# Performance work log

Measured on AMD Instinct MI355X. Metric: run time of the kernel, lower is better.

The kernel has to match this reference:

```python
import jax, jax.numpy as jnp
import numpy as np

B, S, D = 4, 4096, 1024
STATE = 1024
HID = 4 * D
EPS_NORM = 1e-6           # RMSNorm module eps
EPS_FP32 = 1.1920929e-7   # torch F.rms_norm default eps = finfo(fp32).eps


def rms_norm(x, eps):
    # no learned weight (RMSNorm(dim=-1) has weight=None)
    return x * jax.lax.rsqrt(jnp.mean(jnp.square(x), axis=-1, keepdims=True) + eps)


def setup_inputs() -> dict:
    key = jax.random.key(0)
    ks = jax.random.split(key, 8)
    scale_d = 1.0 / np.sqrt(D)
    scale_s = 1.0 / np.sqrt(STATE)
    scale_h = 1.0 / np.sqrt(HID)
    return {
        "x": jax.random.normal(ks[0], (B, S, D), jnp.float32),
        "x0": jax.random.normal(ks[1], (B, S, D), jnp.float32),
        "Wu": jax.random.normal(ks[2], (STATE, D), jnp.float32) * scale_d,
        "Wg": jax.random.normal(ks[3], (STATE, D), jnp.float32) * scale_d,
        "Wo": jax.random.normal(ks[4], (D, STATE), jnp.float32) * scale_s,
        "Wfc": jax.random.normal(ks[5], (HID, D), jnp.float32) * scale_d,
        "Wproj": jax.random.normal(ks[6], (D, HID), jnp.float32) * scale_h,
        "memory_mix": jnp.ones((D,), jnp.float32),
        "mlp_scale": jnp.ones((D,), jnp.float32),
        "resid_mix": jnp.stack([jnp.ones((D,), jnp.float32), jnp.zeros((D,), jnp.float32)]),
    }


def reference(x, x0, Wu, Wg, Wo, Wfc, Wproj, memory_mix, mlp_scale, resid_mix):
    # residual mix of x and x0
    x = resid_mix[0][None, None, :] * x + resid_mix[1][None, None, :] * x0

    # --- CausalPrefixMemory branch ---
    h = rms_norm(x, EPS_NORM)
    update = jnp.einsum('bsd,kd->bsk', h, Wu)
    gate = jax.nn.sigmoid(jnp.einsum('bsd,kd->bsk', h, Wg))
    memory = jnp.cumsum(gate * update, axis=1)          # [B,S,STATE]
    denom = jnp.arange(1, S + 1, dtype=jnp.float32)[None, :, None]
    m = rms_norm(memory / denom, EPS_FP32)
    mem_out = jnp.einsum('bsk,dk->bsd', m, Wo)
    x = x + memory_mix[None, None, :] * mem_out

    # --- MLP branch: relu^2 ---
    h2 = rms_norm(x, EPS_NORM)
    r = jax.nn.relu(jnp.einsum('bsd,hd->bsh', h2, Wfc))
    mlp_out = jnp.einsum('bsh,dh->bsd', jnp.square(r), Wproj)
    x = x + mlp_scale[None, None, :] * mlp_out
    return x
```

## Files before the change

### kernel.cpp

```cpp
#include <hip/hip_runtime.h>
#include <stdint.h>

typedef unsigned short u16;
typedef __attribute__((ext_vector_type(8))) short s16x8;
typedef __attribute__((ext_vector_type(4))) float f32x4;

__device__ __forceinline__ u16 f2bf(float f) {
  uint32_t u = __float_as_uint(f);
  uint32_t r = (u + 0x7FFFu + ((u >> 16) & 1u)) >> 16;
  return (u16)r;
}

__device__ __forceinline__ void gll16(const void* g, void* lds) {
  __builtin_amdgcn_global_load_lds(
      (const __attribute__((address_space(1))) uint32_t*)g,
      (__attribute__((address_space(3))) uint32_t*)lds, 16, 0, 0);
}

__device__ __forceinline__ void xcd_swz(int& bx, int& by) {
  int gx = gridDim.x;
  int lin = blockIdx.y * gx + blockIdx.x;
  int cpx = (gx * gridDim.y) >> 3;
  int nl = (lin & 7) * cpx + (lin >> 3);
  bx = nl % gx;
  by = nl / gx;
}

__global__ __launch_bounds__(256) void k_f2b(const float* __restrict__ src,
                                             u16* __restrict__ dst, int n) {
  int i = (blockIdx.x * 256 + threadIdx.x) * 4;
  if (i < n) {
    float4 v = *(const float4*)(src + i);
    ushort4 o;
    o.x = f2bf(v.x); o.y = f2bf(v.y); o.z = f2bf(v.z); o.w = f2bf(v.w);
    *(ushort4*)(dst + i) = o;
  }
}

template <bool MIX>
__global__ __launch_bounds__(256) void k_rms(const float* __restrict__ X,
                                             const float* __restrict__ X0,
                                             const float* __restrict__ rmix,
                                             float* __restrict__ XMout,
                                             u16* __restrict__ Hout, float eps) {
  const int row = blockIdx.x, t = threadIdx.x;
  const size_t base = (size_t)row * 1024;
  float4 v;
  if (MIX) {
    float4 a = ((const float4*)(X + base))[t];
    float4 b = ((const float4*)(X0 + base))[t];
    float4 c0 = ((const float4*)rmix)[t];
    float4 c1 = ((const float4*)(rmix + 1024))[t];
    v.x = c0.x * a.x + c1.x * b.x;
    v.y = c0.y * a.y + c1.y * b.y;
    v.z = c0.z * a.z + c1.z * b.z;
    v.w = c0.w * a.w + c1.w * b.w;
  } else {
    v = ((const float4*)(X + base))[t];
  }
  float ss = v.x * v.x + v.y * v.y + v.z * v.z + v.w * v.w;
#pragma unroll
  for (int o = 32; o > 0; o >>= 1) ss += __shfl_xor(ss, o);
  __shared__ float red[4];
  if ((t & 63) == 0) red[t >> 6] = ss;
  __syncthreads();
  float tot = red[0] + red[1] + red[2] + red[3];
  float sc = rsqrtf(tot * (1.0f / 1024.0f) + eps);
  if (MIX) ((float4*)(XMout + base))[t] = v;
  ushort4 hv;
  hv.x = f2bf(v.x * sc); hv.y = f2bf(v.y * sc);
  hv.z = f2bf(v.z * sc); hv.w = f2bf(v.w * sc);
  ((ushort4*)(Hout + base))[t] = hv;
}

__global__ __launch_bounds__(256) void k_scan1(const float* __restrict__ P,
                                               float* __restrict__ CS) {
  int blk = blockIdx.x;
  int chunk = blk & 63, b = blk >> 6;
  const float4* p = (const float4*)(P + ((size_t)b * 4096 + chunk * 64) * 1024)
                    + threadIdx.x;
  float4 s = {0.f, 0.f, 0.f, 0.f};
#pragma unroll 8
  for (int i = 0; i < 64; ++i) {
    float4 v = p[(size_t)i * 256];
    s.x += v.x; s.y += v.y; s.z += v.z; s.w += v.w;
  }
  ((float4*)(CS + ((size_t)b * 64 + chunk) * 1024))[threadIdx.x] = s;
}

__global__ __launch_bounds__(256) void k_scan2(float* __restrict__ CS) {
  int idx = blockIdx.x * 256 + threadIdx.x;
  int b = idx >> 10, k = idx & 1023;
  float run = 0.f;
  for (int c = 0; c < 64; ++c) {
    size_t o = ((size_t)b * 64 + c) * 1024 + k;
    float v = CS[o];
    CS[o] = run;
    run += v;
  }
}

__global__ __launch_bounds__(256) void k_scan3f(const float* __restrict__ P,
                                                const float* __restrict__ CS,
                                                u16* __restrict__ Mout) {
  int blk = blockIdx.x;
  int chunk = blk & 63, b = blk >> 6;
  const int t = threadIdx.x, wid = t >> 6;
  __shared__ float red[2][4];
  float4 run = ((const float4*)(CS + ((size_t)b * 64 + chunk) * 1024))[t];
  const float4* p = (const float4*)(P + ((size_t)b * 4096 + chunk * 64) * 1024) + t;
  u16* mo = Mout + ((size_t)b * 4096 + chunk * 64) * 1024 + t * 4;
  for (int i = 0; i < 64; ++i) {
    float4 v = p[(size_t)i * 256];
    run.x += v.x; run.y += v.y; run.z += v.z; run.w += v.w;
    float inv = 1.0f / (float)(chunk * 64 + i + 1);
    float4 y;
    y.x = run.x * inv; y.y = run.y * inv; y.z = run.z * inv; y.w = run.w * inv;
    float ss = y.x * y.x + y.y * y.y + y.z * y.z + y.w * y.w;
#pragma unroll
    for (int o = 32; o > 0; o >>= 1) ss += __shfl_xor(ss, o);
    if ((t & 63) == 0) red[i & 1][wid] = ss;
    __syncthreads();
    float tot = red[i & 1][0] + red[i & 1][1] + red[i & 1][2] + red[i & 1][3];
    float sc = rsqrtf(tot * (1.0f / 1024.0f) + 1.1920929e-7f);
    ushort4 hv;
    hv.x = f2bf(y.x * sc); hv.y = f2bf(y.y * sc);
    hv.z = f2bf(y.z * sc); hv.w = f2bf(y.w * sc);
    *(ushort4*)(mo + (size_t)i * 1024) = hv;
  }
}

__global__ __launch_bounds__(256, 2) void gemm_dual(
    const u16* __restrict__ A, const u16* __restrict__ Bu,
    const u16* __restrict__ Bg, float* __restrict__ P, int K) {
  __shared__ __align__(16) u16 As[128 * 64];
  __shared__ __align__(16) u16 Us[64 * 64];
  __shared__ __align__(16) u16 Gs[64 * 64];
  const int t = threadIdx.x;
  const int lane = t & 63, wid = t >> 6;
  int bx, by;
  xcd_swz(bx, by);
  const int m0 = by * 128, n0 = bx * 64;
  const int wm = wid * 32;
  const int l15 = lane & 15, lhi = lane >> 4;

  size_t gA[4], gU[2];
#pragma unroll
  for (int i = 0; i < 4; ++i) {
    int j = i * 256 + t;
    int row = j >> 3;
    int k16 = (j & 7) ^ (row & 7);
    gA[i] = (size_t)(m0 + row) * K + k16 * 8;
  }
#pragma unroll
  for (int i = 0; i < 2; ++i) {
    int j = i * 256 + t;
    int row = j >> 3;
    int k16 = (j & 7) ^ (row & 7);
    gU[i] = (size_t)(n0 + row) * K + k16 * 8;
  }

  f32x4 au[2][4], ag[2][4];
#pragma unroll
  for (int mi = 0; mi < 2; ++mi)
#pragma unroll
    for (int ni = 0; ni < 4; ++ni) { au[mi][ni] = 0.0f; ag[mi][ni] = 0.0f; }

  for (int kb = 0; kb < K; kb += 64) {
#pragma unroll
    for (int i = 0; i < 4; ++i) {
      int j = i * 256 + t;
      gll16(A + gA[i] + kb, &As[j * 8]);
    }
#pragma unroll
    for (int i = 0; i < 2; ++i) {
      int j = i * 256 + t;
      gll16(Bu + gU[i] + kb, &Us[j * 8]);
      gll16(Bg + gU[i] + kb, &Gs[j * 8]);
    }
    __syncthreads();
#pragma unroll
    for (int kc = 0; kc < 2; ++kc) {
      s16x8 af[2], uf[4], gf[4];
#pragma unroll
      for (int mi = 0; mi < 2; ++mi) {
        int row = wm + mi * 16 + l15;
        int k16 = (kc * 4 + lhi) ^ (row & 7);
        af[mi] = *(const s16x8*)&As[row * 64 + k16 * 8];
      }
#pragma unroll
      for (int ni = 0; ni < 4; ++ni) {
        int row = ni * 16 + l15;
        int k16 = (kc * 4 + lhi) ^ (row & 7);
        uf[ni] = *(const s16x8*)&Us[row * 64 + k16 * 8];
        gf[ni] = *(const s16x8*)&Gs[row * 64 + k16 * 8];
      }
#pragma unroll
      for (int mi = 0; mi < 2; ++mi)
#pragma unroll
        for (int ni = 0; ni < 4; ++ni) {
          au[mi][ni] = __builtin_amdgcn_mfma_f32_16x16x32_bf16(
              af[mi], uf[ni], au[mi][ni], 0, 0, 0);
          ag[mi][ni] = __builtin_amdgcn_mfma_f32_16x16x32_bf16(
              af[mi], gf[ni], ag[mi][ni], 0, 0, 0);
        }
    }
    __syncthreads();
  }

#pragma unroll
  for (int mi = 0; mi < 2; ++mi) {
    int r0 = m0 + wm + mi * 16 + lhi * 4;
#pragma unroll
    for (int ni = 0; ni < 4; ++ni) {
      int c = n0 + ni * 16 + l15;
#pragma unroll
      for (int j = 0; j < 4; ++j) {
        float u = au[mi][ni][j], g = ag[mi][ni][j];
        P[(size_t)(r0 + j) * 1024 + c] = u / (1.0f + __expf(-g));
      }
    }
  }
}

template <int EPI>
__global__ __launch_bounds__(256, 2) void gemm_bf16(
    const u16* __restrict__ A, const u16* __restrict__ Bw, void* __restrict__ Cout,
    const float* __restrict__ Cadd, const float* __restrict__ colscale,
    int K, int lda, int ldb, int ldc) {
  __shared__ __align__(16) u16 As[128 * 64];
  __shared__ __align__(16) u16 Bs[128 * 64];
  const int t = threadIdx.x;
  const int lane = t & 63, wid = t >> 6;
  int bx, by;
  xcd_swz(bx, by);
  const int m0 = by * 128, n0 = bx * 128;
  const int wm = (wid >> 1) * 64, wn = (wid & 1) * 64;
  const int l15 = lane & 15, lhi = lane >> 4;

  size_t gA[4], gB[4];
#pragma unroll
  for (int i = 0; i < 4; ++i) {
    int j = i * 256 + t;
    int row = j >> 3;
    int k16 = (j & 7) ^ (row & 7);
    gA[i] = (size_t)(m0 + row) * lda + k16 * 8;
    gB[i] = (size_t)(n0 + row) * ldb + k16 * 8;
  }

  f32x4 acc[4][4];
#pragma unroll
  for (int mi = 0; mi < 4; ++mi)
#pragma unroll
    for (int ni = 0; ni < 4; ++ni) acc[mi][ni] = 0.0f;

  for (int kb = 0; kb < K; kb += 64) {
#pragma unroll
    for (int i = 0; i < 4; ++i) {
      int j = i * 256 + t;
      gll16(A + gA[i] + kb, &As[j * 8]);
      gll16(Bw + gB[i] + kb, &Bs[j * 8]);
    }
    __syncthreads();
#pragma unroll
    for (int kc = 0; kc < 2; ++kc) {
      s16x8 af[4], bfr[4];
#pragma unroll
      for (int mi = 0; mi < 4; ++mi) {
        int row = wm + mi * 16 + l15;
        int k16 = (kc * 4 + lhi) ^ (row & 7);
        af[mi] = *(const s16x8*)&As[row * 64 + k16 * 8];
      }
#pragma unroll
      for (int ni = 0; ni < 4; ++ni) {
        int row = wn + ni * 16 + l15;
        int k16 = (kc * 4 + lhi) ^ (row & 7);
        bfr[ni] = *(const s16x8*)&Bs[row * 64 + k16 * 8];
      }
#pragma unroll
      for (int mi = 0; mi < 4; ++mi)
#pragma unroll
        for (int ni = 0; ni < 4; ++ni)
          acc[mi][ni] = __builtin_amdgcn_mfma_f32_16x16x32_bf16(
              af[mi], bfr[ni], acc[mi][ni], 0, 0, 0);
    }
    __syncthreads();
  }

#pragma unroll
  for (int mi = 0; mi < 4; ++mi) {
    int r0 = m0 + wm + mi * 16 + lhi * 4;
#pragma unroll
    for (int ni = 0; ni < 4; ++ni) {
      int c = n0 + wn + ni * 16 + l15;
      float cs = (EPI == 1) ? colscale[c] : 0.f;
#pragma unroll
      for (int j = 0; j < 4; ++j) {
        size_t idx = (size_t)(r0 + j) * ldc + c;
        float v = acc[mi][ni][j];
        if (EPI == 1) {
          ((float*)Cout)[idx] = Cadd[idx] + cs * v;
        } else {
          float rv = fmaxf(v, 0.f);
          ((u16*)Cout)[idx] = f2bf(rv * rv);
        }
      }
    }
  }
}

extern "C" void kernel_launch(void* const* d_in, const int* in_sizes, int n_in,
                              void* d_out, int out_size, void* d_ws, size_t ws_size,
                              hipStream_t stream) {
  const float* x = (const float*)d_in[0];
  const float* x0 = (const float*)d_in[1];
  const float* Wu = (const float*)d_in[2];
  const float* Wg = (const float*)d_in[3];
  const float* Wo = (const float*)d_in[4];
  const float* Wfc = (const float*)d_in[5];
  const float* Wpj = (const float*)d_in[6];
  const float* mmix = (const float*)d_in[7];
  const float* mscale = (const float*)d_in[8];
  const float* rmix = (const float*)d_in[9];
  float* out = (float*)d_out;

  const int M = 16384;
  const size_t MiB = 1024 * 1024;

  char* ws = (char*)d_ws;
  u16* WuB = (u16*)ws;   ws += 2 * MiB;
  u16* WgB = (u16*)ws;   ws += 2 * MiB;
  u16* WoB = (u16*)ws;   ws += 2 * MiB;
  u16* WfcB = (u16*)ws;  ws += 8 * MiB;
  u16* WpjB = (u16*)ws;  ws += 8 * MiB;
  u16* h = (u16*)ws;     ws += 32 * MiB;
  char* pool = ws;
  float* P = (float*)pool;
  float* CS = (float*)(pool + 64 * MiB);
  u16* mB = (u16*)(pool + 65 * MiB);
  u16* R2 = (u16*)pool;
  float* xm = out;

  const bool fullR2 = ws_size >= 182 * MiB;

  k_f2b<<<1024, 256, 0, stream>>>(Wu, WuB, 1024 * 1024);
  k_f2b<<<1024, 256, 0, stream>>>(Wg, WgB, 1024 * 1024);
  k_f2b<<<1024, 256, 0, stream>>>(Wo, WoB, 1024 * 1024);
  k_f2b<<<4096, 256, 0, stream>>>(Wfc, WfcB, 4096 * 1024);
  k_f2b<<<4096, 256, 0, stream>>>(Wpj, WpjB, 4096 * 1024);

  k_rms<true><<<M, 256, 0, stream>>>(x, x0, rmix, xm, h, 1e-6f);

  gemm_dual<<<dim3(16, 128), 256, 0, stream>>>(h, WuB, WgB, P, 1024);

  k_scan1<<<256, 256, 0, stream>>>(P, CS);
  k_scan2<<<16, 256, 0, stream>>>(CS);
  k_scan3f<<<256, 256, 0, stream>>>(P, CS, mB);

  gemm_bf16<1><<<dim3(8, 128), 256, 0, stream>>>(mB, WoB, xm, xm, mmix,
                                                 1024, 1024, 1024, 1024);
  k_rms<false><<<M, 256, 0, stream>>>(xm, nullptr, nullptr, nullptr, h, 1e-6f);

  if (fullR2) {
    gemm_bf16<2><<<dim3(32, 128), 256, 0, stream>>>(
        h, WfcB, R2, nullptr, nullptr, 1024, 1024, 1024, 4096);
    gemm_bf16<1><<<dim3(8, 128), 256, 0, stream>>>(
        R2, WpjB, out, out, mscale, 4096, 4096, 4096, 1024);
  } else {
    for (int c = 0; c < 2; ++c) {
      gemm_bf16<2><<<dim3(16, 128), 256, 0, stream>>>(
          h, WfcB + (size_t)c * 2048 * 1024, R2, nullptr, nullptr,
          1024, 1024, 1024, 2048);
      gemm_bf16<1><<<dim3(8, 128), 256, 0, stream>>>(
          R2, WpjB + (size_t)c * 2048, out, out, mscale,
          2048, 2048, 4096, 1024);
    }
  }
}
```

Measured before the change: 532.2 us.

## Split cumsum scan into finer chunks and use one-wave blocks for normalize pass

The chunked prefix-sum over the sequence now uses 256 chunks of 16 rows per batch instead of 64 chunks of 64 rows, so both the chunk-sum and the final scan kernels launch 1024 blocks and fill more of the GPU. The final scan/normalize kernel uses a single 64-thread wavefront per block, with each thread handling four float4 columns. This lets the row RMS reduction finish with shuffles alone and removes the per-row __syncthreads and LDS exchange. In exchange, the serial carry pass over chunk sums is four times longer, and the chunk-sum buffer grows, so the bf16 memory buffer offset moves.

```diff
diff --git a/kernel.cpp b/kernel.cpp
--- a/kernel.cpp
+++ b/kernel.cpp
@@ -76,57 +76,70 @@
 __global__ __launch_bounds__(256) void k_scan1(const float* __restrict__ P,
                                                float* __restrict__ CS) {
   int blk = blockIdx.x;
-  int chunk = blk & 63, b = blk >> 6;
-  const float4* p = (const float4*)(P + ((size_t)b * 4096 + chunk * 64) * 1024)
+  int chunk = blk & 255, b = blk >> 8;
+  const float4* p = (const float4*)(P + ((size_t)b * 4096 + chunk * 16) * 1024)
                     + threadIdx.x;
   float4 s = {0.f, 0.f, 0.f, 0.f};
-#pragma unroll 8
-  for (int i = 0; i < 64; ++i) {
+#pragma unroll
+  for (int i = 0; i < 16; ++i) {
     float4 v = p[(size_t)i * 256];
     s.x += v.x; s.y += v.y; s.z += v.z; s.w += v.w;
   }
-  ((float4*)(CS + ((size_t)b * 64 + chunk) * 1024))[threadIdx.x] = s;
+  ((float4*)(CS + ((size_t)b * 256 + chunk) * 1024))[threadIdx.x] = s;
 }
 
 __global__ __launch_bounds__(256) void k_scan2(float* __restrict__ CS) {
   int idx = blockIdx.x * 256 + threadIdx.x;
   int b = idx >> 10, k = idx & 1023;
   float run = 0.f;
-  for (int c = 0; c < 64; ++c) {
-    size_t o = ((size_t)b * 64 + c) * 1024 + k;
+  for (int c = 0; c < 256; ++c) {
+    size_t o = ((size_t)b * 256 + c) * 1024 + k;
     float v = CS[o];
     CS[o] = run;
     run += v;
   }
 }
 
-__global__ __launch_bounds__(256) void k_scan3f(const float* __restrict__ P,
-                                                const float* __restrict__ CS,
-                                                u16* __restrict__ Mout) {
+__global__ __launch_bounds__(64) void k_scan3f(const float* __restrict__ P,
+                                               const float* __restrict__ CS,
+                                               u16* __restrict__ Mout) {
   int blk = blockIdx.x;
-  int chunk = blk & 63, b = blk >> 6;
-  const int t = threadIdx.x, wid = t >> 6;
-  __shared__ float red[2][4];
-  float4 run = ((const float4*)(CS + ((size_t)b * 64 + chunk) * 1024))[t];
-  const float4* p = (const float4*)(P + ((size_t)b * 4096 + chunk * 64) * 1024) + t;
-  u16* mo = Mout + ((size_t)b * 4096 + chunk * 64) * 1024 + t * 4;
-  for (int i = 0; i < 64; ++i) {
-    float4 v = p[(size_t)i * 256];
-    run.x += v.x; run.y += v.y; run.z += v.z; run.w += v.w;
-    float inv = 1.0f / (float)(chunk * 64 + i + 1);
-    float4 y;
-    y.x = run.x * inv; y.y = run.y * inv; y.z = run.z * inv; y.w = run.w * inv;
-    float ss = y.x * y.x + y.y * y.y + y.z * y.z + y.w * y.w;
+  int chunk = blk & 255, b = blk >> 8;
+  const int t = threadIdx.x;
+  const float4* cs4 = (const float4*)(CS + ((size_t)b * 256 + chunk) * 1024);
+  float4 run[4];
+#pragma unroll
+  for (int q = 0; q < 4; ++q) run[q] = cs4[q * 64 + t];
+  const float4* p4 = (const float4*)(P + ((size_t)b * 4096 + chunk * 16) * 1024);
+  u16* mo = Mout + ((size_t)b * 4096 + chunk * 16) * 1024;
+  const int rowbase = chunk * 16;
+#pragma unroll 2
+  for (int i = 0; i < 16; ++i) {
+    float4 v[4];
+#pragma unroll
+    for (int q = 0; q < 4; ++q) v[q] = p4[(size_t)i * 256 + q * 64 + t];
+    const float inv = 1.0f / (float)(rowbase + i + 1);
+    float4 y[4];
+    float ss = 0.f;
+#pragma unroll
+    for (int q = 0; q < 4; ++q) {
+      run[q].x += v[q].x; run[q].y += v[q].y;
+      run[q].z += v[q].z; run[q].w += v[q].w;
+      y[q].x = run[q].x * inv; y[q].y = run[q].y * inv;
+      y[q].z = run[q].z * inv; y[q].w = run[q].w * inv;
+      ss += y[q].x * y[q].x + y[q].y * y[q].y
+          + y[q].z * y[q].z + y[q].w * y[q].w;
+    }
 #pragma unroll
     for (int o = 32; o > 0; o >>= 1) ss += __shfl_xor(ss, o);
-    if ((t & 63) == 0) red[i & 1][wid] = ss;
-    __syncthreads();
-    float tot = red[i & 1][0] + red[i & 1][1] + red[i & 1][2] + red[i & 1][3];
-    float sc = rsqrtf(tot * (1.0f / 1024.0f) + 1.1920929e-7f);
-    ushort4 hv;
-    hv.x = f2bf(y.x * sc); hv.y = f2bf(y.y * sc);
-    hv.z = f2bf(y.z * sc); hv.w = f2bf(y.w * sc);
-    *(ushort4*)(mo + (size_t)i * 1024) = hv;
+    float sc = rsqrtf(ss * (1.0f / 1024.0f) + 1.1920929e-7f);
+#pragma unroll
+    for (int q = 0; q < 4; ++q) {
+      ushort4 hv;
+      hv.x = f2bf(y[q].x * sc); hv.y = f2bf(y[q].y * sc);
+      hv.z = f2bf(y[q].z * sc); hv.w = f2bf(y[q].w * sc);
+      *(ushort4*)(mo + (size_t)i * 1024 + (q * 64 + t) * 4) = hv;
+    }
   }
 }
 
@@ -337,7 +350,7 @@
   char* pool = ws;
   float* P = (float*)pool;
   float* CS = (float*)(pool + 64 * MiB);
-  u16* mB = (u16*)(pool + 65 * MiB);
+  u16* mB = (u16*)(pool + 68 * MiB);
   u16* R2 = (u16*)pool;
   float* xm = out;
 
@@ -353,9 +366,9 @@
 
   gemm_dual<<<dim3(16, 128), 256, 0, stream>>>(h, WuB, WgB, P, 1024);
 
-  k_scan1<<<256, 256, 0, stream>>>(P, CS);
+  k_scan1<<<1024, 256, 0, stream>>>(P, CS);
   k_scan2<<<16, 256, 0, stream>>>(CS);
-  k_scan3f<<<256, 256, 0, stream>>>(P, CS, mB);
+  k_scan3f<<<1024, 64, 0, stream>>>(P, CS, mB);
 
   gemm_bf16<1><<<dim3(8, 128), 256, 0, stream>>>(mB, WoB, xm, xm, mmix,
                                                  1024, 1024, 1024, 1024);
```

Result: faster. 520.3 us (-2.2%).
